# Performance work log

Hardware: AMD Instinct MI355X
Metric: run time of the kernel (lower is better)

Reference implementation:

```python
import jax, jax.numpy as jnp
import numpy as np

D_MODEL = 1024
N_HEADS = 16
D_HEAD = D_MODEL // N_HEADS
B, L = 4, 2048


def setup_inputs() -> dict:
    key = jax.random.key(0)
    ks = jax.random.split(key, 10)
    s = 1.0 / np.sqrt(D_MODEL)
    inp = {
        "x": jax.random.normal(ks[0], (B, L, D_MODEL), dtype=jnp.float32),
        "src_key_padding_mask": jax.random.randint(ks[1], (B, L), 0, 2) > 0,
        "wq": jax.random.uniform(ks[2], (D_MODEL, D_MODEL), jnp.float32, -s, s),
        "bq": jnp.zeros((D_MODEL,), jnp.float32),
        "wk": jax.random.uniform(ks[3], (D_MODEL, D_MODEL), jnp.float32, -s, s),
        "bk": jnp.zeros((D_MODEL,), jnp.float32),
        "wv": jax.random.uniform(ks[4], (D_MODEL, D_MODEL), jnp.float32, -s, s),
        "bv": jnp.zeros((D_MODEL,), jnp.float32),
        "wo": jax.random.uniform(ks[5], (D_MODEL, D_MODEL), jnp.float32, -s, s),
        "bo": jnp.zeros((D_MODEL,), jnp.float32),
    }
    return inp


def reference(x, src_key_padding_mask, wq, bq, wk, bk, wv, bv, wo, bo):
    # dropout is identity in eval mode
    Bx, Lx, D = x.shape
    H, dh = N_HEADS, D_HEAD

    def proj(w, b):
        # torch nn.Linear: y = x @ w.T + b
        y = jnp.einsum('bld,ed->ble', x, w) + b
        return y.reshape(Bx, Lx, H, dh).transpose(0, 2, 1, 3)  # (B,H,L,dh)

    q = proj(wq, bq)
    k = proj(wk, bk)
    v = proj(wv, bv)

    scores = jnp.einsum('bhqd,bhkd->bhqk', q, k) / jnp.sqrt(jnp.float32(dh))
    scores = jnp.where(src_key_padding_mask[:, None, None, :], jnp.float32(-1e9), scores)
    attn = jax.nn.softmax(scores, axis=-1)
    out = jnp.einsum('bhqk,bhkd->bhqd', attn, v)
    out = out.transpose(0, 2, 1, 3).reshape(Bx, Lx, D)
    out = jnp.einsum('bld,ed->ble', out, wo) + bo
    return out
```

## Files before the change

kernel.cpp:

```cpp
#include <hip/hip_runtime.h>


typedef __attribute__((ext_vector_type(8))) short short8;
typedef __attribute__((ext_vector_type(4))) float f32x4;
typedef __attribute__((ext_vector_type(4))) float floatx4;
typedef __attribute__((ext_vector_type(4))) int int4v;
typedef __attribute__((ext_vector_type(2))) unsigned int u32x2;

#define MFMA16(a, b, c) __builtin_amdgcn_mfma_f32_16x16x32_bf16((a), (b), (c), 0, 0, 0)

__device__ __forceinline__ short f2bf(float f) {
    unsigned u = __float_as_uint(f);
    u += 0x7FFF + ((u >> 16) & 1);
    return (short)(u >> 16);
}

__device__ __forceinline__ float fast_exp2(float x) {
#if __has_builtin(__builtin_amdgcn_exp2f)
    return __builtin_amdgcn_exp2f(x);
#else
    return exp2f(x);
#endif
}

__device__ __forceinline__ void gload_lds16(const short* g, short* l) {
    __builtin_amdgcn_global_load_lds(
        (const __attribute__((address_space(1))) void*)g,
        (__attribute__((address_space(3))) void*)l, 16, 0, 0);
}

__device__ __forceinline__ void cvt8(const float* __restrict__ src,
                                     short* __restrict__ dst, int i) {
    const f32x4* p = (const f32x4*)src + (size_t)i * 2;
    const f32x4 u0 = p[0];
    const f32x4 u1 = p[1];
    short8 s;
    s[0] = f2bf(u0[0]); s[1] = f2bf(u0[1]); s[2] = f2bf(u0[2]); s[3] = f2bf(u0[3]);
    s[4] = f2bf(u1[0]); s[5] = f2bf(u1[1]); s[6] = f2bf(u1[2]); s[7] = f2bf(u1[3]);
    ((short8*)dst)[i] = s;
}

__global__ __launch_bounds__(256) void cvt_kernel(
    const float* __restrict__ src, short* __restrict__ dst, int n8)
{
    const int i = blockIdx.x * 256 + threadIdx.x;
    if (i >= n8) return;
    cvt8(src, dst, i);
}

__global__ __launch_bounds__(256) void cvt3_kernel(
    const float* __restrict__ s0, const float* __restrict__ s1,
    const float* __restrict__ s2, short* __restrict__ d0,
    short* __restrict__ d1, short* __restrict__ d2)
{
    const int which = blockIdx.x >> 9;
    const int i = (blockIdx.x & 511) * 256 + threadIdx.x;
    const float* s = which == 0 ? s0 : which == 1 ? s1 : s2;
    short* d = which == 0 ? d0 : which == 1 ? d1 : d2;
    cvt8(s, d, i);
}

__global__ __launch_bounds__(256) void cvt2_kernel(
    const float* __restrict__ s0, short* __restrict__ d0,
    const float* __restrict__ s1, short* __restrict__ d1)
{
    if (blockIdx.x < 4096) {
        cvt8(s0, d0, blockIdx.x * 256 + threadIdx.x);
    } else {
        cvt8(s1, d1, (blockIdx.x - 4096) * 256 + threadIdx.x);
    }
}

__device__ __forceinline__ void gemm_body(
    const short* __restrict__ A, const short* __restrict__ W,
    const float* __restrict__ bias, void* __restrict__ out,
    int layout, int m0, int n0, float oscale)
{
    __shared__ short As[128 * 32];
    __shared__ short Bs[128 * 32];

    const int t = threadIdx.x;
    const int wave = t >> 6, lane = t & 63;
    const int wm = (wave >> 1) * 64, wn = (wave & 1) * 64;
    const int l15 = lane & 15, quad = lane >> 4;

    const int r4 = lane >> 2;
    const int kc = (lane & 3) * 8;

    short* lA0 = &As[wave * 512 + lane * 8];
    short* lA1 = &As[2048 + wave * 512 + lane * 8];
    short* lB0 = &Bs[wave * 512 + lane * 8];
    short* lB1 = &Bs[2048 + wave * 512 + lane * 8];

    const short* gA0 = A + (size_t)(m0 + wave * 16 + r4) * 1024 + kc;
    const short* gA1 = gA0 + (size_t)64 * 1024;
    const short* gB0 = W + (size_t)(n0 + wave * 16 + r4) * 1024 + kc;
    const short* gB1 = gB0 + (size_t)64 * 1024;

    floatx4 acc[4][4];
#pragma unroll
    for (int i = 0; i < 4; i++)
#pragma unroll
        for (int j = 0; j < 4; j++) {
            acc[i][j][0] = 0.f; acc[i][j][1] = 0.f;
            acc[i][j][2] = 0.f; acc[i][j][3] = 0.f;
        }

    for (int kb = 0; kb < 1024; kb += 32) {
        gload_lds16(gA0 + kb, lA0);
        gload_lds16(gA1 + kb, lA1);
        gload_lds16(gB0 + kb, lB0);
        gload_lds16(gB1 + kb, lB1);
        __syncthreads();

        short8 af[4], bfr[4];
#pragma unroll
        for (int mi = 0; mi < 4; mi++)
            af[mi] = *(short8*)&As[(wm + mi * 16 + l15) * 32 + quad * 8];
#pragma unroll
        for (int ni = 0; ni < 4; ni++)
            bfr[ni] = *(short8*)&Bs[(wn + ni * 16 + l15) * 32 + quad * 8];
#pragma unroll
        for (int mi = 0; mi < 4; mi++)
#pragma unroll
            for (int ni = 0; ni < 4; ni++)
                acc[mi][ni] = MFMA16(af[mi], bfr[ni], acc[mi][ni]);

        __syncthreads();
    }

#pragma unroll
    for (int ni = 0; ni < 4; ni++) {
        const int gn = n0 + wn + ni * 16 + l15;
        const float bv = bias[gn];
#pragma unroll
        for (int mi = 0; mi < 4; mi++) {
#pragma unroll
            for (int r = 0; r < 4; r++) {
                const int gm = m0 + wm + mi * 16 + quad * 4 + r;
                const float v = (acc[mi][ni][r] + bv) * oscale;
                if (layout == 3) {
                    ((float*)out)[(size_t)gm * 1024 + gn] = v;
                } else {
                    const int b = gm >> 11, l = gm & 2047;
                    const int h = gn >> 6,  d = gn & 63;
                    size_t idx;
                    if (layout == 2)
                        idx = ((size_t)(b * 16 + h) * 64 + d) * 2048 + l;
                    else
                        idx = ((size_t)(b * 16 + h) * 2048 + l) * 64 + d;
                    ((short*)out)[idx] = f2bf(v);
                }
            }
        }
    }
}

__global__ __launch_bounds__(256, 3) void qkv_kernel(
    const short* __restrict__ Xb,
    const short* __restrict__ Wq, const short* __restrict__ Wk,
    const short* __restrict__ Wv,
    const float* __restrict__ bq, const float* __restrict__ bk,
    const float* __restrict__ bv,
    short* __restrict__ Qo, short* __restrict__ Ko, short* __restrict__ Vo)
{
    const int chunk = blockIdx.y >> 3;
    const int n0 = (blockIdx.y & 7) * 128;
    const short* W = chunk == 0 ? Wq : chunk == 1 ? Wk : Wv;
    const float* bs = chunk == 0 ? bq : chunk == 1 ? bk : bv;
    void* out = chunk == 0 ? (void*)Qo : chunk == 1 ? (void*)Ko : (void*)Vo;
    const float os = chunk == 0 ? 0.125f * 1.44269504f : 1.0f;
    gemm_body(Xb, W, bs, out, chunk, blockIdx.x * 128, n0, os);
}

__global__ __launch_bounds__(256, 3) void gemm_kernel(
    const short* __restrict__ A, const short* __restrict__ W,
    const float* __restrict__ bias, void* __restrict__ out, int layout)
{
    gemm_body(A, W, bias, out, layout, blockIdx.x * 128, blockIdx.y * 128, 1.0f);
}

__global__ __launch_bounds__(256, 2) void attn_kernel(
    const short* __restrict__ Q, const short* __restrict__ Kc,
    const short* __restrict__ VT, const int* __restrict__ mask,
    float* __restrict__ O)
{
    __shared__ short Plds_all[4][4][16 * 72];

    const int blk = blockIdx.x;
    const int bh = blk & 63;
    const int qg = blk >> 6;
    const int b = bh >> 4, h = bh & 15;
    const int t = threadIdx.x;
    const int wave = t >> 6, lane = t & 63;
    const int l15 = lane & 15, quad = lane >> 4;

    const short* Qb = Q  + (size_t)bh * 2048 * 64;
    const short* Kb = Kc + (size_t)bh * 2048 * 64;
    const short* Vb = VT + (size_t)bh * 64 * 2048;
    const int* mrow = mask + b * 2048;

    const int qbase = qg * 256 + wave * 64;

    short8 aq[4][2];
#pragma unroll
    for (int tt = 0; tt < 4; tt++) {
        const short* qp = Qb + (size_t)(qbase + tt * 16 + l15) * 64 + quad * 8;
        aq[tt][0] = *(const short8*)(qp);
        aq[tt][1] = *(const short8*)(qp + 32);
    }

    short8 vone;
#pragma unroll
    for (int j = 0; j < 8; j++) vone[j] = (short)0x3F80;

    floatx4 accO[4][5];
#pragma unroll
    for (int tt = 0; tt < 4; tt++)
#pragma unroll
        for (int ni = 0; ni < 5; ni++) {
            accO[tt][ni][0] = 0.f; accO[tt][ni][1] = 0.f;
            accO[tt][ni][2] = 0.f; accO[tt][ni][3] = 0.f;
        }

    for (int c0 = 0; c0 < 2048; c0 += 64) {
        short8 kreg[4][2];
#pragma unroll
        for (int g = 0; g < 4; g++) {
            const short* kp = Kb + (size_t)(c0 + g * 16 + l15) * 64 + quad * 8;
            kreg[g][0] = *(const short8*)(kp);
            kreg[g][1] = *(const short8*)(kp + 32);
        }
        f32x4 bias[4];
#pragma unroll
        for (int g = 0; g < 4; g++) {
            const int4v mv = *(const int4v*)&mrow[c0 + g * 16 + quad * 4];
#pragma unroll
            for (int r = 0; r < 4; r++) bias[g][r] = mv[r] ? -1e9f : 0.f;
        }
        short8 vreg[4][2];
#pragma unroll
        for (int ni = 0; ni < 4; ni++) {
            const short* vp = Vb + (size_t)(ni * 16 + l15) * 2048 + c0 + quad * 8;
            vreg[ni][0] = *(const short8*)(vp);
            vreg[ni][1] = *(const short8*)(vp + 32);
        }

#pragma unroll
        for (int tt = 0; tt < 4; tt++) {
            floatx4 s[4];
            __builtin_amdgcn_s_setprio(1);
#pragma unroll
            for (int g = 0; g < 4; g++) {
                floatx4 z = bias[g];
                z = MFMA16(kreg[g][0], aq[tt][0], z);
                s[g] = MFMA16(kreg[g][1], aq[tt][1], z);
            }
            __builtin_amdgcn_s_setprio(0);
            short* Pl = &Plds_all[wave][tt][0];
#pragma unroll
            for (int g = 0; g < 4; g++) {
                const float p0 = fast_exp2(s[g][0]);
                const float p1 = fast_exp2(s[g][1]);
                const float p2 = fast_exp2(s[g][2]);
                const float p3 = fast_exp2(s[g][3]);
                unsigned lo, hi;
                asm("v_cvt_pk_bf16_f32 %0, %1, %2" : "=v"(lo) : "v"(p0), "v"(p1));
                asm("v_cvt_pk_bf16_f32 %0, %1, %2" : "=v"(hi) : "v"(p2), "v"(p3));
                u32x2 w; w[0] = lo; w[1] = hi;
                *(u32x2*)&Pl[l15 * 72 + g * 16 + quad * 4] = w;
            }
        }

        asm volatile("s_waitcnt lgkmcnt(0)" ::: "memory");

#pragma unroll
        for (int tt = 0; tt < 4; tt++) {
            const short* Pl = &Plds_all[wave][tt][0];
            const short8 pa0 = *(const short8*)&Pl[l15 * 72 + quad * 8];
            const short8 pa1 = *(const short8*)&Pl[l15 * 72 + 32 + quad * 8];
            __builtin_amdgcn_s_setprio(1);
#pragma unroll
            for (int ni = 0; ni < 4; ni++) {
                accO[tt][ni] = MFMA16(pa0, vreg[ni][0], accO[tt][ni]);
                accO[tt][ni] = MFMA16(pa1, vreg[ni][1], accO[tt][ni]);
            }
            accO[tt][4] = MFMA16(pa0, vone, accO[tt][4]);
            accO[tt][4] = MFMA16(pa1, vone, accO[tt][4]);
            __builtin_amdgcn_s_setprio(0);
        }
    }

#pragma unroll
    for (int tt = 0; tt < 4; tt++) {
#pragma unroll
        for (int r = 0; r < 4; r++) {
            const float inv = 1.0f / fmaxf(accO[tt][4][r], 1e-30f);
            const int l = qbase + tt * 16 + quad * 4 + r;
#pragma unroll
            for (int ni = 0; ni < 4; ni++) {
                O[(size_t)(b * 2048 + l) * 1024 + h * 64 + ni * 16 + l15] =
                    accO[tt][ni][r] * inv;
            }
        }
    }
}

extern "C" void kernel_launch(void* const* d_in, const int* in_sizes, int n_in,
                              void* d_out, int out_size, void* d_ws, size_t ws_size,
                              hipStream_t stream)
{
    const float* x    = (const float*)d_in[0];
    const int*   mask = (const int*)d_in[1];
    const float* wq   = (const float*)d_in[2];
    const float* bq   = (const float*)d_in[3];
    const float* wk   = (const float*)d_in[4];
    const float* bk   = (const float*)d_in[5];
    const float* wv   = (const float*)d_in[6];
    const float* bv   = (const float*)d_in[7];
    const float* wo   = (const float*)d_in[8];
    const float* bo   = (const float*)d_in[9];
    float* out = (float*)d_out;

    short* Qbuf = (short*)d_ws;
    short* Kbuf = Qbuf + (size_t)8 * 1024 * 1024;
    short* Vt   = Kbuf + (size_t)8 * 1024 * 1024;

    short* Xb  = (short*)d_out;
    short* Wqb = Xb  + (size_t)8 * 1024 * 1024;
    short* Wkb = Wqb + (size_t)1024 * 1024;
    short* Wvb = Wkb + (size_t)1024 * 1024;

    dim3 block(256);

    cvt_kernel<<<dim3(4096), block, 0, stream>>>(x, Xb, 1024 * 1024);
    cvt3_kernel<<<dim3(1536), block, 0, stream>>>(wq, wk, wv, Wqb, Wkb, Wvb);

    qkv_kernel<<<dim3(64, 24), block, 0, stream>>>(
        Xb, Wqb, Wkb, Wvb, bq, bk, bv, Qbuf, Kbuf, Vt);

    attn_kernel<<<dim3(512), block, 0, stream>>>(Qbuf, Kbuf, Vt, mask, out);

    short* Ob  = Qbuf;
    short* Wob = Kbuf;
    cvt2_kernel<<<dim3(4608), block, 0, stream>>>(out, Ob, wo, Wob);

    gemm_kernel<<<dim3(64, 8), block, 0, stream>>>(Ob, Wob, bo, out, 3);
}
```

Baseline: 354.9 us.

## Write attention output as bf16 in head layout and read it directly in output GEMM

The attention kernel now writes its normalized output as bf16 back into the Q buffer in per-head (B,H,L,dh) layout, in place of an fp32 (B,L,D) tensor. The output projection GEMM gains a layout mode that gathers its A operand from that head-major layout, so the separate fp32-to-bf16 conversion pass over the attention output is gone and only Wo is still converted. This removes a full fp32 write plus a read-and-convert pass over 8M elements. The trade-off is extra address arithmetic and strided 128-byte row segments in the GEMM A loads. It also relies on in-place overwrite of Q being safe, which holds because each block only overwrites the Q rows it has already loaded.

```diff
diff --git a/kernel.cpp b/kernel.cpp
--- a/kernel.cpp
+++ b/kernel.cpp
@@ -60,17 +60,6 @@
     cvt8(s, d, i);
 }
 
-__global__ __launch_bounds__(256) void cvt2_kernel(
-    const float* __restrict__ s0, short* __restrict__ d0,
-    const float* __restrict__ s1, short* __restrict__ d1)
-{
-    if (blockIdx.x < 4096) {
-        cvt8(s0, d0, blockIdx.x * 256 + threadIdx.x);
-    } else {
-        cvt8(s1, d1, (blockIdx.x - 4096) * 256 + threadIdx.x);
-    }
-}
-
 __device__ __forceinline__ void gemm_body(
     const short* __restrict__ A, const short* __restrict__ W,
     const float* __restrict__ bias, void* __restrict__ out,
@@ -92,8 +81,17 @@
     short* lB0 = &Bs[wave * 512 + lane * 8];
     short* lB1 = &Bs[2048 + wave * 512 + lane * 8];
 
-    const short* gA0 = A + (size_t)(m0 + wave * 16 + r4) * 1024 + kc;
-    const short* gA1 = gA0 + (size_t)64 * 1024;
+    const short* gA0;
+    const short* gA1;
+    if (layout == 4) {
+        const int mA = m0 + wave * 16 + r4;
+        const int bb = mA >> 11, ll = mA & 2047;
+        gA0 = A + (size_t)bb * 2097152 + (size_t)ll * 64 + kc;
+        gA1 = gA0 + 64 * 64;
+    } else {
+        gA0 = A + (size_t)(m0 + wave * 16 + r4) * 1024 + kc;
+        gA1 = gA0 + (size_t)64 * 1024;
+    }
     const short* gB0 = W + (size_t)(n0 + wave * 16 + r4) * 1024 + kc;
     const short* gB1 = gB0 + (size_t)64 * 1024;
 
@@ -107,8 +105,11 @@
         }
 
     for (int kb = 0; kb < 1024; kb += 32) {
-        gload_lds16(gA0 + kb, lA0);
-        gload_lds16(gA1 + kb, lA1);
+        const size_t aoff = (layout == 4)
+            ? ((size_t)(kb >> 6) * 131072 + (size_t)(kb & 63))
+            : (size_t)kb;
+        gload_lds16(gA0 + aoff, lA0);
+        gload_lds16(gA1 + aoff, lA1);
         gload_lds16(gB0 + kb, lB0);
         gload_lds16(gB1 + kb, lB1);
         __syncthreads();
@@ -139,7 +140,7 @@
             for (int r = 0; r < 4; r++) {
                 const int gm = m0 + wm + mi * 16 + quad * 4 + r;
                 const float v = (acc[mi][ni][r] + bv) * oscale;
-                if (layout == 3) {
+                if (layout >= 3) {
                     ((float*)out)[(size_t)gm * 1024 + gn] = v;
                 } else {
                     const int b = gm >> 11, l = gm & 2047;
@@ -181,21 +182,20 @@
 }
 
 __global__ __launch_bounds__(256, 2) void attn_kernel(
-    const short* __restrict__ Q, const short* __restrict__ Kc,
-    const short* __restrict__ VT, const int* __restrict__ mask,
-    float* __restrict__ O)
+    short* QO, const short* __restrict__ Kc,
+    const short* __restrict__ VT, const int* __restrict__ mask)
 {
     __shared__ short Plds_all[4][4][16 * 72];
 
     const int blk = blockIdx.x;
     const int bh = blk & 63;
     const int qg = blk >> 6;
-    const int b = bh >> 4, h = bh & 15;
+    const int b = bh >> 4;
     const int t = threadIdx.x;
     const int wave = t >> 6, lane = t & 63;
     const int l15 = lane & 15, quad = lane >> 4;
 
-    const short* Qb = Q  + (size_t)bh * 2048 * 64;
+    short* Qb = QO + (size_t)bh * 2048 * 64;
     const short* Kb = Kc + (size_t)bh * 2048 * 64;
     const short* Vb = VT + (size_t)bh * 64 * 2048;
     const int* mrow = mask + b * 2048;
@@ -299,8 +299,8 @@
             const int l = qbase + tt * 16 + quad * 4 + r;
 #pragma unroll
             for (int ni = 0; ni < 4; ni++) {
-                O[(size_t)(b * 2048 + l) * 1024 + h * 64 + ni * 16 + l15] =
-                    accO[tt][ni][r] * inv;
+                Qb[(size_t)l * 64 + ni * 16 + l15] =
+                    f2bf(accO[tt][ni][r] * inv);
             }
         }
     }
@@ -339,11 +339,10 @@
     qkv_kernel<<<dim3(64, 24), block, 0, stream>>>(
         Xb, Wqb, Wkb, Wvb, bq, bk, bv, Qbuf, Kbuf, Vt);
 
-    attn_kernel<<<dim3(512), block, 0, stream>>>(Qbuf, Kbuf, Vt, mask, out);
-
-    short* Ob  = Qbuf;
+    attn_kernel<<<dim3(512), block, 0, stream>>>(Qbuf, Kbuf, Vt, mask);
+
     short* Wob = Kbuf;
-    cvt2_kernel<<<dim3(4608), block, 0, stream>>>(out, Ob, wo, Wob);
-
-    gemm_kernel<<<dim3(64, 8), block, 0, stream>>>(Ob, Wob, bo, out, 3);
-}
+    cvt_kernel<<<dim3(512), block, 0, stream>>>(wo, Wob, 128 * 1024);
+
+    gemm_kernel<<<dim3(64, 8), block, 0, stream>>>(Qbuf, Wob, bo, out, 4);
+}
```

After: 349.6 us. About the same (-1.5%).
